# Optimization experiments

Measured on AMD Instinct MI355X. Metric: run time of the kernel, lower is better.

## Reference

```python
import jax, jax.numpy as jnp
import numpy as np

N, C, H, DH = 4096, 256, 8, 32
E = 32768
MAX_SPD = 3
DEG_B = 8
LN_EPS = 1e-5


def _ln(h, g, b):
    mu = jnp.mean(h, axis=-1, keepdims=True)
    var = jnp.mean((h - mu) ** 2, axis=-1, keepdims=True)
    return g * (h - mu) / jnp.sqrt(var + LN_EPS) + b


def setup_inputs() -> dict:
    key = jax.random.key(0)
    ks = jax.random.split(key, 16)
    s = 1.0 / np.sqrt(C).astype(np.float32)
    s4 = 1.0 / np.sqrt(4 * C).astype(np.float32)
    return {
        "x": jax.random.normal(ks[0], (N, C), jnp.float32),
        "edge_index": jax.random.randint(ks[1], (2, E), 0, N, dtype=jnp.int32),
        "Wq": jax.random.normal(ks[2], (C, C), jnp.float32) * s,
        "bq": jnp.zeros((C,), jnp.float32),
        "Wk": jax.random.normal(ks[3], (C, C), jnp.float32) * s,
        "bk": jnp.zeros((C,), jnp.float32),
        "Wv": jax.random.normal(ks[4], (C, C), jnp.float32) * s,
        "bv": jnp.zeros((C,), jnp.float32),
        "Wo": jax.random.normal(ks[5], (C, C), jnp.float32) * s,
        "bo": jnp.zeros((C,), jnp.float32),
        "W1": jax.random.normal(ks[6], (C, 4 * C), jnp.float32) * s,
        "b1": jnp.zeros((4 * C,), jnp.float32),
        "W2": jax.random.normal(ks[7], (4 * C, C), jnp.float32) * s4,
        "b2": jnp.zeros((C,), jnp.float32),
        "g1": jnp.ones((C,), jnp.float32),
        "beta1": jnp.zeros((C,), jnp.float32),
        "g2": jnp.ones((C,), jnp.float32),
        "beta2": jnp.zeros((C,), jnp.float32),
        # spd_emb is zero-init in torch; use small random so the bias path is exercised
        "spd_emb": jax.random.normal(ks[8], (MAX_SPD + 2, H), jnp.float32) * 0.02,
        "in_deg_emb": jax.random.normal(ks[9], (DEG_B + 1, C), jnp.float32) * 0.02,
        "out_deg_emb": jax.random.normal(ks[10], (DEG_B + 1, C), jnp.float32) * 0.02,
        "et_bias": jax.random.normal(ks[11], (), jnp.float32) * 0.02,
    }


def _bucket(d):
    # floor(log2(d+1)) clamped to [0, DEG_B]
    return jnp.clip(jnp.floor(jnp.log2(d + 1.0)), 0, DEG_B).astype(jnp.int32)


def _spd_buckets(src, dst):
    # use_reverse_spd=True: adjacency A[row=dst, col=src]; anchors = dst, probe = src.
    # Frontier F starts as identity over all nodes (superset of unique-anchor columns;
    # extra columns never probed -> identical result to torch's unique-anchor version).
    F = jnp.eye(N, dtype=jnp.float32)
    spd = jnp.full((E,), MAX_SPD + 1, dtype=jnp.int32)
    unset = jnp.ones((E,), dtype=bool)
    for k in range(1, MAX_SPD + 1):
        # (A @ F) > 0  via edge-gather + per-row max (binary reachability)
        F = (jax.ops.segment_max(F[src], dst, num_segments=N) > 0).astype(jnp.float32)
        reach = F[src, dst] > 0  # probe anchor column dst at row src
        newly = unset & reach
        spd = jnp.where(newly, k, spd)
        unset = unset & ~newly
    return jnp.clip(spd, 1, MAX_SPD + 1)


def reference(x, edge_index, Wq, bq, Wk, bk, Wv, bv, Wo, bo, W1, b1, W2, b2,
              g1, beta1, g2, beta2, spd_emb, in_deg_emb, out_deg_emb, et_bias):
    src, dst = edge_index[0], edge_index[1]
    ones = jnp.ones((E,), jnp.float32)
    in_deg = jax.ops.segment_sum(ones, dst, num_segments=N)
    out_deg = jax.ops.segment_sum(ones, src, num_segments=N)
    x_in = x + in_deg_emb[_bucket(in_deg)] + out_deg_emb[_bucket(out_deg)]

    spd = _spd_buckets(src, dst)  # [E] int in [1, MAX_SPD+1]

    xn = _ln(x_in, g1, beta1)
    Q = (xn @ Wq + bq).reshape(N, H, DH)
    K = (xn @ Wk + bk).reshape(N, H, DH)
    V = (xn @ Wv + bv).reshape(N, H, DH)

    scores = jnp.sum(Q[dst] * K[src], axis=-1) / np.sqrt(DH)  # [E, H]
    scores = scores + spd_emb[spd] + et_bias

    # segment softmax over edges sharing a destination node
    m = jax.ops.segment_max(scores, dst, num_segments=N)  # [N, H]
    m = jnp.where(jnp.isfinite(m), m, 0.0)
    e = jnp.exp(scores - m[dst])
    ssum = jax.ops.segment_sum(e, dst, num_segments=N)
    w = e / jnp.where(ssum[dst] > 0, ssum[dst], 1.0)  # [E, H]

    msg = jax.ops.segment_sum(w[:, :, None] * V[src], dst, num_segments=N)  # [N,H,DH]
    h = x_in + msg.reshape(N, C) @ Wo + bo
    hn = _ln(h, g2, beta2)
    ff = jax.nn.gelu(hn @ W1 + b1, approximate=False) @ W2 + b2
    return h + ff
```

## Files before the change

kernel.cpp:

```cpp
#include <hip/hip_runtime.h>
#include <math.h>

#define NN 4096
#define CC 256
#define HH 8
#define DHD 32
#define EE 32768
#define FW 128
#define MAXD 128

typedef float f32x4 __attribute__((ext_vector_type(4)));
typedef __bf16 bf16x8 __attribute__((ext_vector_type(8)));
typedef __bf16 bf16x4 __attribute__((ext_vector_type(4)));

__device__ __forceinline__ int bucketf(int d){
  float l = log2f((float)d + 1.0f);
  int b = (int)floorf(l);
  return b < 0 ? 0 : (b > 8 ? 8 : b);
}

__global__ void k_deg(const int* __restrict__ src, const int* __restrict__ dst,
                      int* __restrict__ indeg, int* __restrict__ outdeg){
  int e = blockIdx.x*256 + threadIdx.x;
  if(e < EE){
    atomicAdd(&indeg[dst[e]], 1);
    atomicAdd(&outdeg[src[e]], 1);
  }
}

__global__ void k_scan(const int* __restrict__ deg, int* __restrict__ offs){
  __shared__ int part[1024];
  int t = threadIdx.x;
  int v0=deg[t*4], v1=deg[t*4+1], v2=deg[t*4+2], v3=deg[t*4+3];
  int s = v0+v1+v2+v3;
  part[t] = s;
  __syncthreads();
  for(int d=1; d<1024; d<<=1){
    int x = (t>=d) ? part[t-d] : 0;
    __syncthreads();
    part[t] += x;
    __syncthreads();
  }
  int base = (t>0) ? part[t-1] : 0;
  offs[t*4]   = base;
  offs[t*4+1] = base+v0;
  offs[t*4+2] = base+v0+v1;
  offs[t*4+3] = base+v0+v1+v2;
  if(t==1023) offs[4096] = base+s;
}

__global__ void k_scatter(const int* __restrict__ src, const int* __restrict__ dst,
                          const int* __restrict__ offs, int* __restrict__ cursor,
                          int* __restrict__ nsrc){
  int e = blockIdx.x*256+threadIdx.x;
  if(e<EE){
    int d = dst[e], s = src[e];
    int p = atomicAdd(&cursor[d],1);
    nsrc[offs[d]+p] = s;
  }
}

__global__ void k_f1row(const int* __restrict__ offs, const int* __restrict__ nsrc,
                        unsigned* __restrict__ F1){
  int d = blockIdx.x; int w = threadIdx.x;
  int o0 = offs[d], o1 = offs[d+1];
  unsigned v = 0;
  for(int i=o0;i<o1;i++){
    int s = nsrc[i];
    if((s>>5) == w) v |= 1u << (s&31);
  }
  F1[(size_t)d*FW + w] = v;
}

__global__ void k_prop(const int* __restrict__ offs, const int* __restrict__ nsrc,
                       const unsigned* __restrict__ Fin, unsigned* __restrict__ Fout){
  int d = blockIdx.x; int w = threadIdx.x;
  int o0 = offs[d], o1 = offs[d+1];
  unsigned v = 0;
  for(int i=o0;i<o1;i++){
    int s = nsrc[i];
    v |= Fin[(size_t)s*FW + w];
  }
  Fout[(size_t)d*FW + w] = v;
}

__global__ void k_xin_ln(const float* __restrict__ x, const int* __restrict__ indeg,
                         const int* __restrict__ outdeg, const float* __restrict__ iemb,
                         const float* __restrict__ oemb, const float* __restrict__ g,
                         const float* __restrict__ b, float* __restrict__ x_in,
                         __bf16* __restrict__ xn){
  int node = blockIdx.x*4 + (threadIdx.x >> 6);
  int lane = threadIdx.x & 63;
  int bi = bucketf(indeg[node]);
  int bo = bucketf(outdeg[node]);
  float4 xv = ((const float4*)(x + (size_t)node*CC))[lane];
  float4 iv = ((const float4*)(iemb + (size_t)bi*CC))[lane];
  float4 ov = ((const float4*)(oemb + (size_t)bo*CC))[lane];
  float4 v;
  v.x = xv.x+iv.x+ov.x; v.y = xv.y+iv.y+ov.y;
  v.z = xv.z+iv.z+ov.z; v.w = xv.w+iv.w+ov.w;
  ((float4*)(x_in + (size_t)node*CC))[lane] = v;
  float s  = v.x+v.y+v.z+v.w;
  float sq = v.x*v.x+v.y*v.y+v.z*v.z+v.w*v.w;
  #pragma unroll
  for(int m=32;m>=1;m>>=1){ s += __shfl_xor(s,m); sq += __shfl_xor(sq,m); }
  float mu  = s * (1.0f/CC);
  float var = sq * (1.0f/CC) - mu*mu;
  float inv = rsqrtf(var + 1e-5f);
  float4 gv = ((const float4*)g)[lane];
  float4 bv = ((const float4*)b)[lane];
  bf16x4 o;
  o[0] = (__bf16)(gv.x*(v.x-mu)*inv + bv.x);
  o[1] = (__bf16)(gv.y*(v.y-mu)*inv + bv.y);
  o[2] = (__bf16)(gv.z*(v.z-mu)*inv + bv.z);
  o[3] = (__bf16)(gv.w*(v.w-mu)*inv + bv.w);
  *(bf16x4*)(xn + (size_t)node*CC + lane*4) = o;
}

__global__ void k_ln(const float* __restrict__ in, const float* __restrict__ g,
                     const float* __restrict__ b, __bf16* __restrict__ out){
  int node = blockIdx.x*4 + (threadIdx.x >> 6);
  int lane = threadIdx.x & 63;
  float4 v = ((const float4*)(in + (size_t)node*CC))[lane];
  float s  = v.x+v.y+v.z+v.w;
  float sq = v.x*v.x+v.y*v.y+v.z*v.z+v.w*v.w;
  #pragma unroll
  for(int m=32;m>=1;m>>=1){ s += __shfl_xor(s,m); sq += __shfl_xor(sq,m); }
  float mu  = s * (1.0f/CC);
  float var = sq * (1.0f/CC) - mu*mu;
  float inv = rsqrtf(var + 1e-5f);
  float4 gv = ((const float4*)g)[lane];
  float4 bv = ((const float4*)b)[lane];
  bf16x4 o;
  o[0] = (__bf16)(gv.x*(v.x-mu)*inv + bv.x);
  o[1] = (__bf16)(gv.y*(v.y-mu)*inv + bv.y);
  o[2] = (__bf16)(gv.z*(v.z-mu)*inv + bv.z);
  o[3] = (__bf16)(gv.w*(v.w-mu)*inv + bv.w);
  *(bf16x4*)(out + (size_t)node*CC + lane*4) = o;
}

__global__ void k_pre(const float* __restrict__ Wq, const float* __restrict__ Wk,
                      const float* __restrict__ Wv, const float* __restrict__ Wo,
                      const float* __restrict__ W1, const float* __restrict__ W2,
                      const float* __restrict__ bq, const float* __restrict__ bk,
                      const float* __restrict__ bv,
                      __bf16* __restrict__ WqkvT, __bf16* __restrict__ WoT,
                      __bf16* __restrict__ W1T, __bf16* __restrict__ W2T,
                      float* __restrict__ bqkv, int* __restrict__ zero_base){
  int b = blockIdx.x;
  int tid = threadIdx.x;
  if(b >= 193){
    zero_base[(b-193)*256 + tid] = 0;
    return;
  }
  if(b == 192){
    bqkv[tid]     = bq[tid];
    bqkv[256+tid] = bk[tid];
    bqkv[512+tid] = bv[tid];
    return;
  }
  const float* W; __bf16* Wt; int K, N, tile;
  if(b < 16)      { W=Wq; Wt=WqkvT;        K=256;  N=256;  tile=b; }
  else if(b < 32) { W=Wk; Wt=WqkvT+65536;  K=256;  N=256;  tile=b-16; }
  else if(b < 48) { W=Wv; Wt=WqkvT+131072; K=256;  N=256;  tile=b-32; }
  else if(b < 64) { W=Wo; Wt=WoT;          K=256;  N=256;  tile=b-48; }
  else if(b < 128){ W=W1; Wt=W1T;          K=256;  N=1024; tile=b-64; }
  else            { W=W2; Wt=W2T;          K=1024; N=256;  tile=b-128; }
  int nK = K/64;
  int tk = tile % nK, tn = tile / nK;
  __shared__ float T[64][65];
  int c = tid & 63, r0 = tid >> 6;
  #pragma unroll
  for(int i=0;i<16;i++){
    int row = r0*16 + i;
    T[row][c] = W[(size_t)(tk*64+row)*N + tn*64 + c];
  }
  __syncthreads();
  #pragma unroll
  for(int i=0;i<16;i++){
    int row = r0*16 + i;
    Wt[(size_t)(tn*64+row)*K + tk*64 + c] = (__bf16)T[c][row];
  }
}

template<int MODE>
__global__ __launch_bounds__(256) void k_bgemm(const __bf16* __restrict__ A, const __bf16* __restrict__ Bt,
                       const float* __restrict__ bias, const float* __restrict__ add,
                       float* __restrict__ outf, __bf16* __restrict__ outb,
                       int M, int N, int K){
  __shared__ __bf16 As[64*64];
  __shared__ __bf16 Bs[64*64];
  const int tid = threadIdx.x;
  const int lane = tid & 63, w = tid >> 6;
  const int wr = w >> 1, wc = w & 1;
  const int l15 = lane & 15, g = lane >> 4;
  const int bm = blockIdx.y*64, bn = blockIdx.x*64;
  f32x4 acc[2][2] = {};
  for(int k0=0; k0<K; k0+=64){
    #pragma unroll
    for(int rep=0; rep<2; rep++){
      int q = tid + rep*256;
      int row = q>>3, cb = (q&7)*16;
      int byte_ = row*128 + cb; byte_ ^= (row&7)<<4;
      *(bf16x8*)((char*)As + byte_) = *(const bf16x8*)(A  + (size_t)(bm+row)*K + k0 + (q&7)*8);
      *(bf16x8*)((char*)Bs + byte_) = *(const bf16x8*)(Bt + (size_t)(bn+row)*K + k0 + (q&7)*8);
    }
    __syncthreads();
    #pragma unroll
    for(int ks=0; ks<2; ks++){
      bf16x8 a[2], b[2];
      #pragma unroll
      for(int i=0;i<2;i++){
        int row = wr*32 + i*16 + l15;
        int byte_ = row*128 + ks*64 + g*16; byte_ ^= (row&7)<<4;
        a[i] = *(const bf16x8*)((const char*)As + byte_);
      }
      #pragma unroll
      for(int j=0;j<2;j++){
        int row = wc*32 + j*16 + l15;
        int byte_ = row*128 + ks*64 + g*16; byte_ ^= (row&7)<<4;
        b[j] = *(const bf16x8*)((const char*)Bs + byte_);
      }
      #pragma unroll
      for(int i=0;i<2;i++)
        #pragma unroll
        for(int j=0;j<2;j++)
          acc[i][j] = __builtin_amdgcn_mfma_f32_16x16x32_bf16(a[i], b[j], acc[i][j], 0, 0, 0);
    }
    __syncthreads();
  }
  #pragma unroll
  for(int i=0;i<2;i++){
    #pragma unroll
    for(int j=0;j<2;j++){
      int col = bn + wc*32 + j*16 + l15;
      float bv = bias[col];
      #pragma unroll
      for(int r=0;r<4;r++){
        int rowg = bm + wr*32 + i*16 + g*4 + r;
        float v = acc[i][j][r] + bv;
        if(MODE==1) v += add[(size_t)rowg*N + col];
        if(MODE==2){
          v = 0.5f*v*(1.0f + erff(v*0.70710678118654752f));
          outb[(size_t)rowg*N + col] = (__bf16)v;
        } else if(MODE==3){
          outb[(size_t)rowg*N + col] = (__bf16)v;
        } else {
          outf[(size_t)rowg*N + col] = v;
        }
      }
    }
  }
}

__global__ void k_sagg(const int* __restrict__ nsrc, const int* __restrict__ offs,
                       const __bf16* __restrict__ QKV,
                       const unsigned* __restrict__ F1, const unsigned* __restrict__ F2,
                       const unsigned* __restrict__ F3,
                       const float* __restrict__ spde, __bf16* __restrict__ msg){
  __shared__ float scs[MAXD][9];
  __shared__ int   sl[MAXD];
  __shared__ int   spi[MAXD];
  const int d = blockIdx.x;
  const int t = threadIdx.x;
  const int o0 = offs[d];
  int deg = offs[d+1] - o0; if(deg > MAXD) deg = MAXD;
  if(t < deg){
    int s = nsrc[o0+t];
    sl[t] = s;
    size_t wi = (size_t)s*FW + (d>>5); unsigned bb = 1u << (d&31);
    int sp = 4;
    if(F3[wi] & bb) sp = 3;
    if(F2[wi] & bb) sp = 2;
    if(F1[wi] & bb) sp = 1;
    spi[t] = sp;
  }
  __syncthreads();
  { const int h = t & 7, i0 = t >> 3;
    const bf16x8* qr = (const bf16x8*)(QKV + (size_t)d*768 + h*DHD);
    for(int i=i0; i<deg; i+=32){
      const bf16x8* kr = (const bf16x8*)(QKV + (size_t)sl[i]*768 + 256 + h*DHD);
      float acc = 0.f;
      #pragma unroll
      for(int j=0;j<4;j++){
        bf16x8 kv = kr[j], qv = qr[j];
        #pragma unroll
        for(int u=0;u<8;u++) acc += (float)qv[u] * (float)kv[u];
      }
      scs[i][h] = acc * 0.17677669529663687f + spde[spi[i]*HH + h];
    }
  }
  __syncthreads();
  { const int h = t >> 5, l = t & 31;
    float m = -3.0e38f;
    for(int i=l;i<deg;i+=32) m = fmaxf(m, scs[i][h]);
    #pragma unroll
    for(int mk=16;mk>=1;mk>>=1) m = fmaxf(m, __shfl_xor(m,mk));
    float ss = 0.f;
    for(int i=l;i<deg;i+=32) ss += expf(scs[i][h]-m);
    #pragma unroll
    for(int mk=16;mk>=1;mk>>=1) ss += __shfl_xor(ss,mk);
    float inv = (ss>0.f) ? 1.f/ss : 1.f;
    for(int i=l;i<deg;i+=32) scs[i][h] = expf(scs[i][h]-m)*inv;
  }
  __syncthreads();
  { const int h = t >> 5, c = t & 31;
    float acc = 0.f;
    for(int i=0;i<deg;i++)
      acc += scs[i][h] * (float)QKV[(size_t)sl[i]*768 + 512 + h*DHD + c];
    msg[(size_t)d*CC + h*DHD + c] = (__bf16)acc;
  }
}

extern "C" void kernel_launch(void* const* d_in, const int* in_sizes, int n_in,
                              void* d_out, int out_size, void* d_ws, size_t ws_size,
                              hipStream_t stream){
  const float* x  = (const float*)d_in[0];
  const int*  ei  = (const int*)d_in[1];
  const float* Wq = (const float*)d_in[2];  const float* bq = (const float*)d_in[3];
  const float* Wk = (const float*)d_in[4];  const float* bk = (const float*)d_in[5];
  const float* Wv = (const float*)d_in[6];  const float* bv = (const float*)d_in[7];
  const float* Wo = (const float*)d_in[8];  const float* bo = (const float*)d_in[9];
  const float* W1 = (const float*)d_in[10]; const float* b1 = (const float*)d_in[11];
  const float* W2 = (const float*)d_in[12]; const float* b2 = (const float*)d_in[13];
  const float* g1 = (const float*)d_in[14]; const float* be1= (const float*)d_in[15];
  const float* g2 = (const float*)d_in[16]; const float* be2= (const float*)d_in[17];
  const float* spde = (const float*)d_in[18];
  const float* iemb = (const float*)d_in[19];
  const float* oemb = (const float*)d_in[20];
  const float* etb  = (const float*)d_in[21]; (void)etb;
  const int* src = ei;
  const int* dst = ei + EE;
  float* out = (float*)d_out;

  const size_t NC = (size_t)NN*CC;
  float* ws   = (float*)d_ws;
  float* x_in = ws;
  float* hbuf = ws + NC;
  int* indeg  = (int*)(ws + 2*NC);
  int* outdeg = indeg + NN;
  int* cursor = outdeg + NN;
  unsigned* F1 = (unsigned*)(cursor + NN);
  unsigned* F2 = F1 + (size_t)NN*FW;
  unsigned* F3 = F2 + (size_t)NN*FW;
  __bf16* QKV  = (__bf16*)(F3 + (size_t)NN*FW);
  __bf16* xn_bf  = (__bf16*)(ws + 5517312);
  __bf16* msg_bf = (__bf16*)(ws + 6041600);
  __bf16* WqkvT  = (__bf16*)(ws + 6565888);
  __bf16* WoT    = WqkvT + 196608;
  __bf16* W1T    = WoT + 65536;
  __bf16* W2T    = W1T + 262144;
  float* bqkv    = ws + 6959104;
  int* offs      = (int*)(bqkv + 768);
  int* nsrc      = offs + NN + 4;
  __bf16* ff1_bf = (__bf16*)(ws + 2*NC);
  __bf16* hn_bf  = (__bf16*)(ws + 4*NC);

  k_pre<<<241,256,0,stream>>>(Wq,Wk,Wv,Wo,W1,W2,bq,bk,bv,WqkvT,WoT,W1T,W2T,bqkv,indeg);
  k_deg<<<EE/256,256,0,stream>>>(src,dst,indeg,outdeg);
  k_scan<<<1,1024,0,stream>>>(indeg,offs);
  k_scatter<<<EE/256,256,0,stream>>>(src,dst,offs,cursor,nsrc);
  k_f1row<<<NN,FW,0,stream>>>(offs,nsrc,F1);
  k_prop<<<NN,FW,0,stream>>>(offs,nsrc,F1,F2);
  k_prop<<<NN,FW,0,stream>>>(offs,nsrc,F2,F3);
  k_xin_ln<<<NN/4,256,0,stream>>>(x,indeg,outdeg,iemb,oemb,g1,be1,x_in,xn_bf);

  dim3 gq(768/64, NN/64);
  k_bgemm<3><<<gq,256,0,stream>>>(xn_bf, WqkvT, bqkv, nullptr, nullptr, QKV, NN, 768, 256);

  k_sagg<<<NN,256,0,stream>>>(nsrc,offs,QKV,F1,F2,F3,spde,msg_bf);

  dim3 go(256/64, NN/64);
  k_bgemm<1><<<go,256,0,stream>>>(msg_bf, WoT, bo, x_in, hbuf, nullptr, NN, 256, 256);
  k_ln <<<NN/4,256,0,stream>>>(hbuf,g2,be2,hn_bf);
  dim3 gf1(1024/64, NN/64);
  k_bgemm<2><<<gf1,256,0,stream>>>(hn_bf, W1T, b1, nullptr, nullptr, ff1_bf, NN, 1024, 256);
  dim3 gf2(256/64, NN/64);
  k_bgemm<1><<<gf2,256,0,stream>>>(ff1_bf, W2T, b2, hbuf, out, nullptr, NN, 256, 1024);
}
```

Measured before the change: 94.47 us.

## Enlarge GEMM M-tile to 128 and merge F1 build with input LayerNorm

The bf16 MFMA GEMM now uses 128x64 tiles, with each wave computing a 64x32 sub-tile (4x2 MFMA accumulators). This raises A/B reuse per LDS load and halves the number of blocks. Separately, the F1 adjacency-bitmap build and the x_in/LayerNorm kernel are merged into one launch, with the block index selecting the role, to save a launch and let the two run concurrently. The risk is that the smaller grids (e.g. 128 blocks for the N=256 GEMMs) may underfill the 256 CUs on MI355X, and the extra accumulators raise register pressure.

Measured after the change: 101.3 us. 7.2% more time.

```diff
diff --git a/kernel.cpp b/kernel.cpp
--- a/kernel.cpp
+++ b/kernel.cpp
@@ -60,37 +60,29 @@
   }
 }
 
-__global__ void k_f1row(const int* __restrict__ offs, const int* __restrict__ nsrc,
-                        unsigned* __restrict__ F1){
-  int d = blockIdx.x; int w = threadIdx.x;
-  int o0 = offs[d], o1 = offs[d+1];
-  unsigned v = 0;
-  for(int i=o0;i<o1;i++){
-    int s = nsrc[i];
-    if((s>>5) == w) v |= 1u << (s&31);
-  }
-  F1[(size_t)d*FW + w] = v;
-}
-
-__global__ void k_prop(const int* __restrict__ offs, const int* __restrict__ nsrc,
-                       const unsigned* __restrict__ Fin, unsigned* __restrict__ Fout){
-  int d = blockIdx.x; int w = threadIdx.x;
-  int o0 = offs[d], o1 = offs[d+1];
-  unsigned v = 0;
-  for(int i=o0;i<o1;i++){
-    int s = nsrc[i];
-    v |= Fin[(size_t)s*FW + w];
-  }
-  Fout[(size_t)d*FW + w] = v;
-}
-
-__global__ void k_xin_ln(const float* __restrict__ x, const int* __restrict__ indeg,
-                         const int* __restrict__ outdeg, const float* __restrict__ iemb,
-                         const float* __restrict__ oemb, const float* __restrict__ g,
-                         const float* __restrict__ b, float* __restrict__ x_in,
-                         __bf16* __restrict__ xn){
-  int node = blockIdx.x*4 + (threadIdx.x >> 6);
-  int lane = threadIdx.x & 63;
+__global__ void k_mid(const int* __restrict__ offs, const int* __restrict__ nsrc,
+                      unsigned* __restrict__ F1,
+                      const float* __restrict__ x, const int* __restrict__ indeg,
+                      const int* __restrict__ outdeg, const float* __restrict__ iemb,
+                      const float* __restrict__ oemb, const float* __restrict__ g,
+                      const float* __restrict__ be, float* __restrict__ x_in,
+                      __bf16* __restrict__ xn){
+  int b = blockIdx.x;
+  int tid = threadIdx.x;
+  if(b < 2048){
+    int d = b*2 + (tid>>7);
+    int w = tid & 127;
+    int o0 = offs[d], o1 = offs[d+1];
+    unsigned v = 0;
+    for(int i=o0;i<o1;i++){
+      int s = nsrc[i];
+      if((s>>5) == w) v |= 1u << (s&31);
+    }
+    F1[(size_t)d*FW + w] = v;
+    return;
+  }
+  int node = (b-2048)*4 + (tid >> 6);
+  int lane = tid & 63;
   int bi = bucketf(indeg[node]);
   int bo = bucketf(outdeg[node]);
   float4 xv = ((const float4*)(x + (size_t)node*CC))[lane];
@@ -108,13 +100,25 @@
   float var = sq * (1.0f/CC) - mu*mu;
   float inv = rsqrtf(var + 1e-5f);
   float4 gv = ((const float4*)g)[lane];
-  float4 bv = ((const float4*)b)[lane];
+  float4 bv = ((const float4*)be)[lane];
   bf16x4 o;
   o[0] = (__bf16)(gv.x*(v.x-mu)*inv + bv.x);
   o[1] = (__bf16)(gv.y*(v.y-mu)*inv + bv.y);
   o[2] = (__bf16)(gv.z*(v.z-mu)*inv + bv.z);
   o[3] = (__bf16)(gv.w*(v.w-mu)*inv + bv.w);
   *(bf16x4*)(xn + (size_t)node*CC + lane*4) = o;
+}
+
+__global__ void k_prop(const int* __restrict__ offs, const int* __restrict__ nsrc,
+                       const unsigned* __restrict__ Fin, unsigned* __restrict__ Fout){
+  int d = blockIdx.x; int w = threadIdx.x;
+  int o0 = offs[d], o1 = offs[d+1];
+  unsigned v = 0;
+  for(int i=o0;i<o1;i++){
+    int s = nsrc[i];
+    v |= Fin[(size_t)s*FW + w];
+  }
+  Fout[(size_t)d*FW + w] = v;
 }
 
 __global__ void k_ln(const float* __restrict__ in, const float* __restrict__ g,
@@ -188,30 +192,36 @@
                        const float* __restrict__ bias, const float* __restrict__ add,
                        float* __restrict__ outf, __bf16* __restrict__ outb,
                        int M, int N, int K){
-  __shared__ __bf16 As[64*64];
+  __shared__ __bf16 As[128*64];
   __shared__ __bf16 Bs[64*64];
   const int tid = threadIdx.x;
   const int lane = tid & 63, w = tid >> 6;
   const int wr = w >> 1, wc = w & 1;
   const int l15 = lane & 15, g = lane >> 4;
-  const int bm = blockIdx.y*64, bn = blockIdx.x*64;
-  f32x4 acc[2][2] = {};
+  const int bm = blockIdx.y*128, bn = blockIdx.x*64;
+  f32x4 acc[4][2] = {};
   for(int k0=0; k0<K; k0+=64){
+    #pragma unroll
+    for(int rep=0; rep<4; rep++){
+      int q = tid + rep*256;
+      int row = q>>3;
+      int byte_ = row*128 + (q&7)*16; byte_ ^= (row&7)<<4;
+      *(bf16x8*)((char*)As + byte_) = *(const bf16x8*)(A + (size_t)(bm+row)*K + k0 + (q&7)*8);
+    }
     #pragma unroll
     for(int rep=0; rep<2; rep++){
       int q = tid + rep*256;
-      int row = q>>3, cb = (q&7)*16;
-      int byte_ = row*128 + cb; byte_ ^= (row&7)<<4;
-      *(bf16x8*)((char*)As + byte_) = *(const bf16x8*)(A  + (size_t)(bm+row)*K + k0 + (q&7)*8);
+      int row = q>>3;
+      int byte_ = row*128 + (q&7)*16; byte_ ^= (row&7)<<4;
       *(bf16x8*)((char*)Bs + byte_) = *(const bf16x8*)(Bt + (size_t)(bn+row)*K + k0 + (q&7)*8);
     }
     __syncthreads();
     #pragma unroll
     for(int ks=0; ks<2; ks++){
-      bf16x8 a[2], b[2];
-      #pragma unroll
-      for(int i=0;i<2;i++){
-        int row = wr*32 + i*16 + l15;
+      bf16x8 a[4], b[2];
+      #pragma unroll
+      for(int i=0;i<4;i++){
+        int row = wr*64 + i*16 + l15;
         int byte_ = row*128 + ks*64 + g*16; byte_ ^= (row&7)<<4;
         a[i] = *(const bf16x8*)((const char*)As + byte_);
       }
@@ -222,7 +232,7 @@
         b[j] = *(const bf16x8*)((const char*)Bs + byte_);
       }
       #pragma unroll
-      for(int i=0;i<2;i++)
+      for(int i=0;i<4;i++)
         #pragma unroll
         for(int j=0;j<2;j++)
           acc[i][j] = __builtin_amdgcn_mfma_f32_16x16x32_bf16(a[i], b[j], acc[i][j], 0, 0, 0);
@@ -230,14 +240,14 @@
     __syncthreads();
   }
   #pragma unroll
-  for(int i=0;i<2;i++){
+  for(int i=0;i<4;i++){
     #pragma unroll
     for(int j=0;j<2;j++){
       int col = bn + wc*32 + j*16 + l15;
       float bv = bias[col];
       #pragma unroll
       for(int r=0;r<4;r++){
-        int rowg = bm + wr*32 + i*16 + g*4 + r;
+        int rowg = bm + wr*64 + i*16 + g*4 + r;
         float v = acc[i][j][r] + bv;
         if(MODE==1) v += add[(size_t)rowg*N + col];
         if(MODE==2){
@@ -360,21 +370,20 @@
   k_deg<<<EE/256,256,0,stream>>>(src,dst,indeg,outdeg);
   k_scan<<<1,1024,0,stream>>>(indeg,offs);
   k_scatter<<<EE/256,256,0,stream>>>(src,dst,offs,cursor,nsrc);
-  k_f1row<<<NN,FW,0,stream>>>(offs,nsrc,F1);
+  k_mid<<<3072,256,0,stream>>>(offs,nsrc,F1,x,indeg,outdeg,iemb,oemb,g1,be1,x_in,xn_bf);
   k_prop<<<NN,FW,0,stream>>>(offs,nsrc,F1,F2);
   k_prop<<<NN,FW,0,stream>>>(offs,nsrc,F2,F3);
-  k_xin_ln<<<NN/4,256,0,stream>>>(x,indeg,outdeg,iemb,oemb,g1,be1,x_in,xn_bf);
-
-  dim3 gq(768/64, NN/64);
+
+  dim3 gq(768/64, NN/128);
   k_bgemm<3><<<gq,256,0,stream>>>(xn_bf, WqkvT, bqkv, nullptr, nullptr, QKV, NN, 768, 256);
 
   k_sagg<<<NN,256,0,stream>>>(nsrc,offs,QKV,F1,F2,F3,spde,msg_bf);
 
-  dim3 go(256/64, NN/64);
+  dim3 go(256/64, NN/128);
   k_bgemm<1><<<go,256,0,stream>>>(msg_bf, WoT, bo, x_in, hbuf, nullptr, NN, 256, 256);
   k_ln <<<NN/4,256,0,stream>>>(hbuf,g2,be2,hn_bf);
-  dim3 gf1(1024/64, NN/64);
+  dim3 gf1(1024/64, NN/128);
   k_bgemm<2><<<gf1,256,0,stream>>>(hn_bf, W1T, b1, nullptr, nullptr, ff1_bf, NN, 1024, 256);
-  dim3 gf2(256/64, NN/64);
+  dim3 gf2(256/64, NN/128);
   k_bgemm<1><<<gf2,256,0,stream>>>(ff1_bf, W2T, b2, hbuf, out, nullptr, NN, 256, 1024);
 }
```
